# Kernel tuning notes

Hardware: AMD Instinct MI355X
Metric: run time of the kernel (lower is better)

The kernel has to match this reference:

```python
import jax, jax.numpy as jnp
import numpy as np

N = 100000      # nodes
E = 1200000     # edges (every node gets >=1 incoming edge)
DIN = 64
DOUT = 64
EDIM = 16
AVG_D = 2.5649493574615367  # log(avg_in_degree + 1) = log(13)
EPS = 1e-5


def setup_inputs() -> dict:
    key = jax.random.key(0)
    ks = jax.random.split(key, 10)
    h = jax.random.normal(ks[0], (N, DIN), dtype=jnp.float32)
    e = jax.random.normal(ks[1], (E, EDIM), dtype=jnp.float32)
    snorm_n = jax.random.uniform(ks[2], (N, 1), dtype=jnp.float32, minval=0.05, maxval=1.0)
    src = jax.random.randint(ks[3], (E,), 0, N, dtype=jnp.int32)
    # guarantee in-degree >= 1 for every node (DGL reduce requires non-empty mailbox)
    dst = jnp.concatenate([jnp.arange(N, dtype=jnp.int32),
                           jax.random.randint(ks[4], (E - N,), 0, N, dtype=jnp.int32)])
    d_pre_in = 2 * DIN + EDIM  # 144
    d_post_in = (4 * 3 + 1) * DIN  # 832
    W_pre = jax.random.normal(ks[5], (d_pre_in, DIN), dtype=jnp.float32) / np.sqrt(d_pre_in)
    b_pre = jnp.zeros((DIN,), dtype=jnp.float32)
    W_post = jax.random.normal(ks[6], (d_post_in, DOUT), dtype=jnp.float32) / np.sqrt(d_post_in)
    b_post = jnp.zeros((DOUT,), dtype=jnp.float32)
    bn_gamma = jnp.ones((DOUT,), dtype=jnp.float32)
    bn_beta = jnp.zeros((DOUT,), dtype=jnp.float32)
    return {"h": h, "e": e, "snorm_n": snorm_n,
            "W_pre": W_pre, "b_pre": b_pre, "W_post": W_post, "b_post": b_post,
            "bn_gamma": bn_gamma, "bn_beta": bn_beta, "src": src, "dst": dst}


def reference(h, e, snorm_n, W_pre, b_pre, W_post, b_post, bn_gamma, bn_beta, src, dst):
    n = h.shape[0]
    # --- pretrans on edges: MLP(cat[src_feat, dst_feat, edge_feat]) (1 layer, no act) ---
    z = jnp.concatenate([h[src], h[dst], e], axis=1)           # [E, 2*DIN+EDIM]
    m = z @ W_pre + b_pre                                      # [E, DIN] edge messages
    # --- multi-aggregator segment reduce over destination mailboxes ---
    deg = jax.ops.segment_sum(jnp.ones((m.shape[0],), m.dtype), dst, num_segments=n)
    D = deg[:, None]                                           # [N,1], all >= 1
    s1 = jax.ops.segment_sum(m, dst, num_segments=n)
    s2 = jax.ops.segment_sum(m * m, dst, num_segments=n)
    mean = s1 / D
    std = jnp.sqrt(jax.nn.relu(s2 / D - mean * mean) + EPS)
    mx = jax.ops.segment_max(m, dst, num_segments=n)
    mn = jax.ops.segment_min(m, dst, num_segments=n)
    agg = jnp.concatenate([mean, mx, mn, std], axis=1)          # [N, 4*DIN]
    # --- degree scalers: identity, amplification, attenuation ---
    logd = jnp.log(D + 1.0)
    scaled = jnp.concatenate([agg, agg * (logd / AVG_D), agg * (AVG_D / logd)], axis=1)  # [N, 12*DIN]
    # --- posttrans on cat[h, aggregated] (1 layer, no act) ---
    feat = jnp.concatenate([h, scaled], axis=1)                 # [N, 13*DIN]
    out = feat @ W_post + b_post                                # [N, DOUT]
    out = out * snorm_n                                        # graph norm
    # BatchNorm1d in training mode (batch stats over nodes, biased var)
    mu = out.mean(axis=0)
    var = out.var(axis=0)
    out = (out - mu) / jnp.sqrt(var + 1e-5) * bn_gamma + bn_beta
    # dropout p=0.0 -> identity
    return out
```

## Files before the change

### kernel.cpp

```cpp
#include <hip/hip_runtime.h>
#include <hip/hip_bf16.h>
#include <math.h>

#define N_NODES 100000
#define N_EDGES 1200000
#define NT_EDGE 75000
#define NPASS   3
#define TILES_PER_PASS 25000
#define ROWS_PER_PASS  400000
#define NT_POST 6250
#define AVG_D   2.5649493574615367f
#define EPSV    1e-5f

typedef __attribute__((ext_vector_type(8))) short short8;
typedef __attribute__((ext_vector_type(4))) float f32x4;

struct ERec { unsigned eid, sn, dn; };

#define OFF_DEG       0u
#define OFF_ROWLOCAL  400000u
#define OFF_BSUM      800000u
#define OFF_BOFFS     802048u
#define OFF_ROWSTART  804096u
#define OFF_CURSOR    1204096u
#define OFF_EREC      1604096u
#define OFF_AB        16004096u
#define OFF_BNACC     16804096u
#define OFF_BNFIN     16804608u
#define OFF_HB        16805120u
#define OFF_MBUF      29605120u
#define OFF_AGG       80805120u
#define OFF_WFRAG     132005120u
#define OFF_WFRAG2    132025600u
#define OFF_CARRY     OFF_BSUM
#define OFF_OUTPRE    OFF_MBUF

__device__ __forceinline__ short f2b(float f){
    union { float f; unsigned u; } c; c.f = f;
    unsigned u = c.u;
    unsigned r = (u + 0x7fffu + ((u >> 16) & 1u)) >> 16;
    return (short)r;
}
__device__ __forceinline__ float b2f(unsigned u16){
    union { unsigned u; float f; } c; c.u = u16 << 16;
    return c.f;
}
__device__ __forceinline__ unsigned pk(float a, float b){
    return ((unsigned)(unsigned short)f2b(a)) | (((unsigned)(unsigned short)f2b(b)) << 16);
}

__global__ void k_prep(const int* __restrict__ dst, unsigned* __restrict__ deg,
                       const float* __restrict__ h, unsigned short* __restrict__ hb,
                       const float* __restrict__ W_pre, unsigned short* __restrict__ wfrag,
                       const float* __restrict__ W_post, unsigned short* __restrict__ wfrag2){
    int i = blockIdx.x*256 + threadIdx.x;
    if (i < N_EDGES) atomicAdd(&deg[dst[i]], 1u);
    if (i < 800000){
        const float4* p = (const float4*)h + (size_t)i*2;
        float4 u0 = p[0], u1 = p[1];
        uint4 o;
        o.x = pk(u0.x,u0.y); o.y = pk(u0.z,u0.w);
        o.z = pk(u1.x,u1.y); o.w = pk(u1.z,u1.w);
        ((uint4*)hb)[i] = o;
    }
    if (i < 10240){
        int e = i & 7, l = (i>>3) & 63, q = i>>9;
        int ks = q>>2, cg = q&3;
        int lr = l&15, lg = l>>4;
        int k = ks*32 + lg*8 + e, col = cg*16 + lr;
        wfrag[i] = (unsigned short)((k < 144) ? f2b(W_pre[k*64 + col]) : (short)0);
    }
    if (i < 53248){
        int e = i & 7, l = (i>>3) & 63, g = i>>9;
        int cg = g & 3, f = g>>2;
        int lr = l&15, lg = l>>4;
        int col = cg*16 + lr;
        int row;
        if      (f < 10) row = f*32        + lg*8 + e;
        else if (f < 18) row = 320 + (f-10)*32 + lg*8 + e;
        else             row = 576 + (f-18)*32 + lg*8 + e;
        wfrag2[i] = (unsigned short)f2b(W_post[row*64 + col]);
    }
}
__global__ void k_scan1(const unsigned* __restrict__ deg, unsigned* __restrict__ rowlocal,
                        unsigned* __restrict__ bsum){
    __shared__ unsigned s[256];
    int t = threadIdx.x; int i = blockIdx.x*256 + t;
    unsigned d = (i < N_NODES) ? deg[i] : 0u;
    s[t] = d; __syncthreads();
    for (int off=1; off<256; off<<=1){
        unsigned v = (t>=off) ? s[t-off] : 0u; __syncthreads();
        s[t] += v; __syncthreads();
    }
    if (i < N_NODES) rowlocal[i] = s[t] - d;
    if (t == 255) bsum[blockIdx.x] = s[255];
}
__global__ void k_scan2(const unsigned* __restrict__ bsum, unsigned* __restrict__ boffs){
    __shared__ unsigned s[512];
    int t = threadIdx.x;
    unsigned v = (t < 391) ? bsum[t] : 0u;
    s[t] = v; __syncthreads();
    for (int off=1; off<512; off<<=1){
        unsigned x = (t>=off) ? s[t-off] : 0u; __syncthreads();
        s[t] += x; __syncthreads();
    }
    boffs[t] = s[t] - v;
}
__global__ void k_scan3(const unsigned* __restrict__ rowlocal, const unsigned* __restrict__ boffs,
                        unsigned* __restrict__ rowstart){
    int i = blockIdx.x*256 + threadIdx.x;
    if (i < N_NODES) rowstart[i] = rowlocal[i] + boffs[i>>8];
}
__global__ void k_scatter(const int* __restrict__ src, const int* __restrict__ dst,
                          const unsigned* __restrict__ rowstart,
                          unsigned* __restrict__ cursor, ERec* __restrict__ erec){
    int i = blockIdx.x*256 + threadIdx.x;
    if (i < N_EDGES){
        int d = dst[i];
        int s = src[i];
        unsigned pos = rowstart[d] + atomicAdd(&cursor[d], 1u);
        unsigned* p = (unsigned*)&erec[pos];
        __builtin_nontemporal_store((unsigned)i, p);
        __builtin_nontemporal_store((unsigned)s, p+1);
        __builtin_nontemporal_store((unsigned)d, p+2);
    }
}

__global__ __launch_bounds__(256) void k_edge(
    const unsigned short* __restrict__ hb, const float* __restrict__ e_in,
    const unsigned short* __restrict__ wfrag, const float* __restrict__ b_pre,
    const ERec* __restrict__ erec, unsigned short* __restrict__ mbuf, int pass)
{
    __shared__ __align__(16) uint4 wfl[1280];
    int tid = threadIdx.x;
    int wv = tid>>6, l = tid&63;
    int lr = l&15, lg = l>>4;

    int t = blockIdx.x*4 + wv;
    const ERec* er = erec + (size_t)pass*ROWS_PER_PASS;
    ERec r = er[(size_t)t*16 + lr];

    for (int j=tid; j<1280; j+=256) wfl[j] = ((const uint4*)wfrag)[j];
    __syncthreads();

    const unsigned short* ps = hb + (size_t)r.sn*64 + lg*8;
    const unsigned short* pd = hb + (size_t)r.dn*64 + lg*8;
    short8 A[5];
    A[0] = *(const short8*)ps;
    A[1] = *(const short8*)(ps + 32);
    A[2] = *(const short8*)pd;
    A[3] = *(const short8*)(pd + 32);
    {
        short8 A4 = {0,0,0,0,0,0,0,0};
        if (lg < 2){
            const float* pe = e_in + (size_t)r.eid*16 + lg*8;
            float4 u0 = *(const float4*)pe, u1 = *(const float4*)(pe+4);
            A4[0]=f2b(u0.x); A4[1]=f2b(u0.y); A4[2]=f2b(u0.z); A4[3]=f2b(u0.w);
            A4[4]=f2b(u1.x); A4[5]=f2b(u1.y); A4[6]=f2b(u1.z); A4[7]=f2b(u1.w);
        }
        A[4] = A4;
    }

    f32x4 acc[4];
    #pragma unroll
    for (int cg=0; cg<4; cg++) acc[cg] = (f32x4){0.f,0.f,0.f,0.f};
    #pragma unroll
    for (int ks=0; ks<5; ks++){
        #pragma unroll
        for (int cg=0; cg<4; cg++){
            short8 b = ((const short8*)wfl)[(ks*4+cg)*64 + l];
            acc[cg] = __builtin_amdgcn_mfma_f32_16x16x32_bf16(A[ks], b, acc[cg], 0,0,0);
        }
    }
    float bias[4];
    #pragma unroll
    for (int cg=0; cg<4; cg++) bias[cg] = b_pre[cg*16 + lr];
    #pragma unroll
    for (int rr=0; rr<4; rr++){
        size_t row = (size_t)t*16 + lg*4 + rr;
        #pragma unroll
        for (int cg=0; cg<4; cg++)
            mbuf[row*64 + cg*16 + lr] = (unsigned short)f2b(acc[cg][rr] + bias[cg]);
    }
}

__global__ __launch_bounds__(256) void k_agg(
    const unsigned short* __restrict__ mbuf, const unsigned* __restrict__ rowstart,
    const unsigned* __restrict__ deg, unsigned short* __restrict__ agg,
    float* __restrict__ ab, float* __restrict__ carry, int pass)
{
    int wv = threadIdx.x>>6, l = threadIdx.x&63;
    int node = blockIdx.x*4 + wv;
    int hf = l>>5, c = l&31;
    unsigned start = rowstart[node];
    int d = (int)deg[node];
    unsigned end = start + (unsigned)d;
    unsigned lo = (unsigned)pass * ROWS_PER_PASS;
    unsigned hi = lo + ROWS_PER_PASS;
    if (end <= lo || start >= hi) return;
    unsigned a = start < lo ? lo : start;
    unsigned b = end > hi ? hi : end;
    int n = (int)(b - a);
    const unsigned short* p = mbuf + (size_t)(a - lo)*64 + 2*c;
    float s1a=0.f,s2a=0.f,mxa=-3.402823466e38f,mna=3.402823466e38f;
    float s1b=0.f,s2b=0.f,mxb=-3.402823466e38f,mnb=3.402823466e38f;
    for (int i=hf; i<n; i+=2){
        unsigned v = *(const unsigned*)(p + (size_t)i*64);
        float va = b2f(v & 0xffffu), vb = b2f(v >> 16);
        s1a += va; s2a = fmaf(va,va,s2a); mxa = fmaxf(mxa,va); mna = fminf(mna,va);
        s1b += vb; s2b = fmaf(vb,vb,s2b); mxb = fmaxf(mxb,vb); mnb = fminf(mnb,vb);
    }
    s1a += __shfl_xor(s1a,32); s2a += __shfl_xor(s2a,32);
    mxa = fmaxf(mxa,__shfl_xor(mxa,32)); mna = fminf(mna,__shfl_xor(mna,32));
    s1b += __shfl_xor(s1b,32); s2b += __shfl_xor(s2b,32);
    mxb = fmaxf(mxb,__shfl_xor(mxb,32)); mnb = fminf(mnb,__shfl_xor(mnb,32));
    if (l < 32){
        if (start < lo){
            const float* cb = carry + (size_t)(pass-1)*256;
            s1a += cb[      2*c];   s1b += cb[      2*c+1];
            s2a += cb[ 64 + 2*c];   s2b += cb[ 64 + 2*c+1];
            mxa = fmaxf(mxa, cb[128 + 2*c]); mxb = fmaxf(mxb, cb[128 + 2*c+1]);
            mna = fminf(mna, cb[192 + 2*c]); mnb = fminf(mnb, cb[192 + 2*c+1]);
        }
        if (end > hi){
            float* cb = carry + (size_t)pass*256;
            cb[      2*c] = s1a;  cb[      2*c+1] = s1b;
            cb[ 64 + 2*c] = s2a;  cb[ 64 + 2*c+1] = s2b;
            cb[128 + 2*c] = mxa;  cb[128 + 2*c+1] = mxb;
            cb[192 + 2*c] = mna;  cb[192 + 2*c+1] = mnb;
        } else {
            float D = (float)d;
            float meana = s1a/D, meanb = s1b/D;
            float sda = sqrtf(fmaxf(s2a/D - meana*meana, 0.f) + EPSV);
            float sdb = sqrtf(fmaxf(s2b/D - meanb*meanb, 0.f) + EPSV);
            unsigned* ag = (unsigned*)(agg + (size_t)node*256) + c;
            ag[ 0] = pk(meana, meanb);
            ag[32] = pk(mxa,  mxb);
            ag[64] = pk(mna,  mnb);
            ag[96] = pk(sda,  sdb);
            if (c == 0){
                float logd = logf(D + 1.f);
                ab[node*2]   = logd / AVG_D;
                ab[node*2+1] = AVG_D / logd;
            }
        }
    }
}

__global__ __launch_bounds__(256) void k_post(
    const unsigned short* __restrict__ hb, const unsigned short* __restrict__ agg,
    const unsigned short* __restrict__ wfrag2,
    const float* __restrict__ ab, const float* __restrict__ snorm,
    const float* __restrict__ b_post,
    float* __restrict__ out_pre, float* __restrict__ bn_acc)
{
    int tid = threadIdx.x;
    int cg = tid>>6;
    int l = tid&63, lr = l&15, lg = l>>4;
    int col = cg*16 + lr;

    const short8* wf = (const short8*)wfrag2;
    short8 Bm[10], B2[8], B3[8];
    #pragma unroll
    for (int ks=0; ks<10; ks++) Bm[ks] = wf[(ks*4      + cg)*64 + l];
    #pragma unroll
    for (int ks=0; ks<8; ks++){
        B2[ks] = wf[((10+ks)*4 + cg)*64 + l];
        B3[ks] = wf[((18+ks)*4 + cg)*64 + l];
    }
    float bias = b_post[col];
    float bs = 0.f, bq = 0.f;

    for (int t = blockIdx.x; t < NT_POST; t += gridDim.x){
        int nodeA = t*16 + lr;
        f32x4 aM = {0.f,0.f,0.f,0.f}, a2 = {0.f,0.f,0.f,0.f}, a3 = {0.f,0.f,0.f,0.f};
        #pragma unroll
        for (int ks=0; ks<2; ks++){
            short8 A = *(const short8*)(hb + (size_t)nodeA*64 + ks*32 + lg*8);
            aM = __builtin_amdgcn_mfma_f32_16x16x32_bf16(A, Bm[ks], aM, 0,0,0);
        }
        #pragma unroll
        for (int ks=0; ks<8; ks++){
            short8 A = *(const short8*)(agg + (size_t)nodeA*256 + ks*32 + lg*8);
            aM = __builtin_amdgcn_mfma_f32_16x16x32_bf16(A, Bm[2+ks], aM, 0,0,0);
            a2 = __builtin_amdgcn_mfma_f32_16x16x32_bf16(A, B2[ks],  a2, 0,0,0);
            a3 = __builtin_amdgcn_mfma_f32_16x16x32_bf16(A, B3[ks],  a3, 0,0,0);
        }
        #pragma unroll
        for (int r=0; r<4; r++){
            int node = t*16 + lg*4 + r;
            float av = ab[node*2], bv = ab[node*2+1];
            float v = (aM[r] + av*a2[r] + bv*a3[r] + bias) * snorm[node];
            out_pre[(size_t)node*64 + col] = v;
            bs += v; bq = fmaf(v,v,bq);
        }
    }
    bs += __shfl_xor(bs, 16); bs += __shfl_xor(bs, 32);
    bq += __shfl_xor(bq, 16); bq += __shfl_xor(bq, 32);
    if (l < 16){
        atomicAdd(&bn_acc[cg*16 + l], bs);
        atomicAdd(&bn_acc[64 + cg*16 + l], bq);
    }
}

__global__ void k_bnfin(const float* __restrict__ bn_acc, const float* __restrict__ gamma,
                        const float* __restrict__ beta, float* __restrict__ bn_fin){
    int c = threadIdx.x;
    float invN = 1.f/(float)N_NODES;
    float mu = bn_acc[c]*invN;
    float ms = bn_acc[64+c]*invN;
    float var = fmaxf(ms - mu*mu, 0.f);
    float scale = gamma[c] / sqrtf(var + 1e-5f);
    bn_fin[c] = scale;
    bn_fin[64+c] = beta[c] - mu*scale;
}
__global__ void k_apply(const float* __restrict__ out_pre, const float* __restrict__ bn_fin,
                        float* __restrict__ out){
    int i = blockIdx.x*256 + threadIdx.x;
    int c4 = (i & 15) * 4;
    float4 v  = ((const float4*)out_pre)[i];
    float4 sc = *(const float4*)&bn_fin[c4];
    float4 sh = *(const float4*)&bn_fin[64 + c4];
    float4 o;
    o.x = fmaf(v.x, sc.x, sh.x); o.y = fmaf(v.y, sc.y, sh.y);
    o.z = fmaf(v.z, sc.z, sh.z); o.w = fmaf(v.w, sc.w, sh.w);
    ((float4*)out)[i] = o;
}

extern "C" void kernel_launch(void* const* d_in, const int* in_sizes, int n_in,
                              void* d_out, int out_size, void* d_ws, size_t ws_size,
                              hipStream_t stream)
{
    const float* h      = (const float*)d_in[0];
    const float* e_in   = (const float*)d_in[1];
    const float* snorm  = (const float*)d_in[2];
    const float* W_pre  = (const float*)d_in[3];
    const float* b_pre  = (const float*)d_in[4];
    const float* W_post = (const float*)d_in[5];
    const float* b_post = (const float*)d_in[6];
    const float* gamma  = (const float*)d_in[7];
    const float* beta   = (const float*)d_in[8];
    const int*   src    = (const int*)d_in[9];
    const int*   dst    = (const int*)d_in[10];

    char* ws = (char*)d_ws;
    unsigned* deg      = (unsigned*)(ws + OFF_DEG);
    unsigned* rowlocal = (unsigned*)(ws + OFF_ROWLOCAL);
    unsigned* bsum     = (unsigned*)(ws + OFF_BSUM);
    unsigned* boffs    = (unsigned*)(ws + OFF_BOFFS);
    unsigned* rowstart = (unsigned*)(ws + OFF_ROWSTART);
    unsigned* cursor   = (unsigned*)(ws + OFF_CURSOR);
    ERec*     erec     = (ERec*)(ws + OFF_EREC);
    float*    abuf     = (float*)(ws + OFF_AB);
    float*    bnacc    = (float*)(ws + OFF_BNACC);
    float*    bnfin    = (float*)(ws + OFF_BNFIN);
    unsigned short* hb     = (unsigned short*)(ws + OFF_HB);
    unsigned short* mbuf   = (unsigned short*)(ws + OFF_MBUF);
    unsigned short* aggp   = (unsigned short*)(ws + OFF_AGG);
    unsigned short* wfrag  = (unsigned short*)(ws + OFF_WFRAG);
    unsigned short* wfrag2 = (unsigned short*)(ws + OFF_WFRAG2);
    float*    carry    = (float*)(ws + OFF_CARRY);
    float*    outpre   = (float*)(ws + OFF_OUTPRE);

    hipMemsetAsync(ws + OFF_DEG,    0, 400000, stream);
    hipMemsetAsync(ws + OFF_CURSOR, 0, 400000, stream);
    hipMemsetAsync(ws + OFF_BNACC,  0, 512,    stream);

    k_prep   <<<4688, 256, 0, stream>>>(dst, deg, h, hb, W_pre, wfrag, W_post, wfrag2);
    k_scan1  <<<391,  256, 0, stream>>>(deg, rowlocal, bsum);
    k_scan2  <<<1,    512, 0, stream>>>(bsum, boffs);
    k_scan3  <<<391,  256, 0, stream>>>(rowlocal, boffs, rowstart);
    k_scatter<<<4688, 256, 0, stream>>>(src, dst, rowstart, cursor, erec);

    for (int pass = 0; pass < NPASS; pass++){
        k_edge <<<6250, 256, 0, stream>>>(hb, e_in, wfrag, b_pre, erec, mbuf, pass);
        k_agg  <<<25000,256, 0, stream>>>(mbuf, rowstart, deg, aggp, abuf, carry, pass);
    }

    k_post   <<<1024, 256, 0, stream>>>(hb, aggp, wfrag2, abuf, snorm, b_post, outpre, bnacc);
    k_bnfin  <<<1,    64,  0, stream>>>(bnacc, gamma, beta, bnfin);
    k_apply  <<<6250, 256, 0, stream>>>(outpre, bnfin, (float*)d_out);
}
```

Baseline: 535.8 us.

## Replace atomic CSR scatter with two-level bucketed binning and LDS placement

Splits the edge-to-CSR scatter into two steps. The first bins edges into 512-node destination buckets using LDS histograms and one global atomic per bucket per block. The second places each bucket's edges into final CSR slots using LDS cursors. This replaces 1.2M global atomics and scattered 12-byte writes with mostly local atomics and more coalesced writes, at the cost of an extra pass through a staging buffer. Edge order within each node becomes nondeterministic, as it was before.

```diff
diff --git a/kernel.cpp b/kernel.cpp
--- a/kernel.cpp
+++ b/kernel.cpp
@@ -11,6 +11,10 @@
 #define NT_POST 6250
 #define AVG_D   2.5649493574615367f
 #define EPSV    1e-5f
+
+#define BUK_SHIFT 9
+#define NBUK 196
+#define EB_PER_BLOCK 4096
 
 typedef __attribute__((ext_vector_type(8))) short short8;
 typedef __attribute__((ext_vector_type(4))) float f32x4;
@@ -33,6 +37,7 @@
 #define OFF_WFRAG     132005120u
 #define OFF_WFRAG2    132025600u
 #define OFF_CARRY     OFF_BSUM
+#define OFF_STAGING   OFF_MBUF
 #define OFF_OUTPRE    OFF_MBUF
 
 __device__ __forceinline__ short f2b(float f){
@@ -107,22 +112,71 @@
     boffs[t] = s[t] - v;
 }
 __global__ void k_scan3(const unsigned* __restrict__ rowlocal, const unsigned* __restrict__ boffs,
-                        unsigned* __restrict__ rowstart){
+                        unsigned* __restrict__ rowstart, unsigned* __restrict__ bukCursor){
     int i = blockIdx.x*256 + threadIdx.x;
-    if (i < N_NODES) rowstart[i] = rowlocal[i] + boffs[i>>8];
-}
-__global__ void k_scatter(const int* __restrict__ src, const int* __restrict__ dst,
-                          const unsigned* __restrict__ rowstart,
-                          unsigned* __restrict__ cursor, ERec* __restrict__ erec){
-    int i = blockIdx.x*256 + threadIdx.x;
-    if (i < N_EDGES){
-        int d = dst[i];
-        int s = src[i];
-        unsigned pos = rowstart[d] + atomicAdd(&cursor[d], 1u);
-        unsigned* p = (unsigned*)&erec[pos];
-        __builtin_nontemporal_store((unsigned)i, p);
-        __builtin_nontemporal_store((unsigned)s, p+1);
-        __builtin_nontemporal_store((unsigned)d, p+2);
+    if (i < N_NODES){
+        unsigned v = rowlocal[i] + boffs[i>>8];
+        rowstart[i] = v;
+        if ((i & 511) == 0) bukCursor[i>>BUK_SHIFT] = v;
+    }
+}
+
+__global__ __launch_bounds__(256) void k_bin(
+    const int* __restrict__ src, const int* __restrict__ dst,
+    unsigned* __restrict__ bukCursor, ERec* __restrict__ staging)
+{
+    __shared__ unsigned hist[NBUK];
+    __shared__ unsigned gbase[NBUK];
+    int tid = threadIdx.x;
+    for (int j=tid; j<NBUK; j+=256) hist[j]=0u;
+    __syncthreads();
+    int base = blockIdx.x*EB_PER_BLOCK;
+    int sn[16], dn[16];
+    #pragma unroll
+    for (int k=0;k<16;k++){
+        int i = base + k*256 + tid;
+        if (i < N_EDGES){
+            sn[k]=src[i]; dn[k]=dst[i];
+            atomicAdd(&hist[dn[k]>>BUK_SHIFT],1u);
+        } else dn[k] = -1;
+    }
+    __syncthreads();
+    for (int j=tid; j<NBUK; j+=256){
+        unsigned c = hist[j];
+        gbase[j] = c ? atomicAdd(&bukCursor[j], c) : 0u;
+        hist[j] = 0u;
+    }
+    __syncthreads();
+    #pragma unroll
+    for (int k=0;k<16;k++){
+        int i = base + k*256 + tid;
+        if (i < N_EDGES){
+            int b = dn[k]>>BUK_SHIFT;
+            unsigned off = atomicAdd(&hist[b],1u);
+            ERec r; r.eid=(unsigned)i; r.sn=(unsigned)sn[k]; r.dn=(unsigned)dn[k];
+            staging[gbase[b]+off] = r;
+        }
+    }
+}
+
+__global__ __launch_bounds__(256) void k_place(
+    const ERec* __restrict__ staging, const unsigned* __restrict__ rowstart,
+    ERec* __restrict__ erec)
+{
+    __shared__ unsigned cur[512];
+    int b = blockIdx.x;
+    int nbase = b<<BUK_SHIFT;
+    int nend  = nbase + 512; if (nend > N_NODES) nend = N_NODES;
+    int tid = threadIdx.x;
+    for (int j=tid; j<512; j+=256)
+        cur[j] = (nbase+j < N_NODES) ? rowstart[nbase+j] : (unsigned)N_EDGES;
+    __syncthreads();
+    unsigned p0 = rowstart[nbase];
+    unsigned p1 = (nend < N_NODES) ? rowstart[nend] : (unsigned)N_EDGES;
+    for (unsigned p = p0 + tid; p < p1; p += 256){
+        ERec r = staging[p];
+        unsigned pos = atomicAdd(&cur[r.dn - nbase], 1u);
+        erec[pos] = r;
     }
 }
 
@@ -349,8 +403,9 @@
     unsigned* bsum     = (unsigned*)(ws + OFF_BSUM);
     unsigned* boffs    = (unsigned*)(ws + OFF_BOFFS);
     unsigned* rowstart = (unsigned*)(ws + OFF_ROWSTART);
-    unsigned* cursor   = (unsigned*)(ws + OFF_CURSOR);
+    unsigned* bukCur   = (unsigned*)(ws + OFF_CURSOR);
     ERec*     erec     = (ERec*)(ws + OFF_EREC);
+    ERec*     staging  = (ERec*)(ws + OFF_STAGING);
     float*    abuf     = (float*)(ws + OFF_AB);
     float*    bnacc    = (float*)(ws + OFF_BNACC);
     float*    bnfin    = (float*)(ws + OFF_BNFIN);
@@ -362,15 +417,15 @@
     float*    carry    = (float*)(ws + OFF_CARRY);
     float*    outpre   = (float*)(ws + OFF_OUTPRE);
 
-    hipMemsetAsync(ws + OFF_DEG,    0, 400000, stream);
-    hipMemsetAsync(ws + OFF_CURSOR, 0, 400000, stream);
-    hipMemsetAsync(ws + OFF_BNACC,  0, 512,    stream);
+    hipMemsetAsync(ws + OFF_DEG,   0, 400000, stream);
+    hipMemsetAsync(ws + OFF_BNACC, 0, 512,    stream);
 
     k_prep   <<<4688, 256, 0, stream>>>(dst, deg, h, hb, W_pre, wfrag, W_post, wfrag2);
     k_scan1  <<<391,  256, 0, stream>>>(deg, rowlocal, bsum);
     k_scan2  <<<1,    512, 0, stream>>>(bsum, boffs);
-    k_scan3  <<<391,  256, 0, stream>>>(rowlocal, boffs, rowstart);
-    k_scatter<<<4688, 256, 0, stream>>>(src, dst, rowstart, cursor, erec);
+    k_scan3  <<<391,  256, 0, stream>>>(rowlocal, boffs, rowstart, bukCur);
+    k_bin    <<<293,  256, 0, stream>>>(src, dst, bukCur, staging);
+    k_place  <<<NBUK, 256, 0, stream>>>(staging, rowstart, erec);
 
     for (int pass = 0; pass < NPASS; pass++){
         k_edge <<<6250, 256, 0, stream>>>(hb, e_in, wfrag, b_pre, erec, mbuf, pass);
```

Result: faster. 479.5 us (-10.5%).
